# Kernel optimization log

Hardware: AMD Instinct MI355X
Metric: run time of the kernel (lower is better)

## Reference

```python
import jax, jax.numpy as jnp
import numpy as np

B, N_Z, NOISE_DIM, STATE_DIM, HIDDEN_DIM, CLASS_NUM = 2048, 8, 32, 1024, 1024, 1
EPI_HIDDEN = 512
PRIOR_H = 5
IN_FEATURES = NOISE_DIM + STATE_DIM + HIDDEN_DIM  # 2080
OUT_FEATURES = NOISE_DIM * CLASS_NUM  # 32
POSTERIOR_SCALE = 1.0
PRIOR_SCALE = 1.0


def _xavier(key, shape):
    fan_in, fan_out = shape[-2], shape[-1]
    std = np.sqrt(2.0 / (fan_in + fan_out)).astype(np.float32)
    return jax.random.normal(key, shape, dtype=jnp.float32) * std


def setup_inputs() -> dict:
    key = jax.random.key(0)
    ks = jax.random.split(key, 10)
    x = jax.random.normal(ks[0], (B, STATE_DIM), dtype=jnp.float32)
    feature = jax.random.normal(ks[1], (B, HIDDEN_DIM), dtype=jnp.float32)
    z = jax.random.normal(ks[2], (B, N_Z, NOISE_DIM), dtype=jnp.float32)
    # epinet: Linear(IN_FEATURES->EPI_HIDDEN), ReLU, Linear(EPI_HIDDEN->OUT_FEATURES)
    Wep1 = _xavier(ks[3], (IN_FEATURES, EPI_HIDDEN))
    bep1 = jnp.zeros((EPI_HIDDEN,), dtype=jnp.float32)
    Wep2 = _xavier(ks[4], (EPI_HIDDEN, OUT_FEATURES))
    bep2 = jnp.zeros((OUT_FEATURES,), dtype=jnp.float32)
    # priornet: ensemble of NOISE_DIM MLPs state_dim->5->5->class_num (frozen)
    Wp1 = _xavier(ks[5], (NOISE_DIM, STATE_DIM, PRIOR_H))
    bp1 = jnp.zeros((NOISE_DIM, PRIOR_H), dtype=jnp.float32)
    Wp2 = _xavier(ks[6], (NOISE_DIM, PRIOR_H, PRIOR_H))
    bp2 = jnp.zeros((NOISE_DIM, PRIOR_H), dtype=jnp.float32)
    Wp3 = _xavier(ks[7], (NOISE_DIM, PRIOR_H, CLASS_NUM))
    bp3 = jnp.zeros((NOISE_DIM, CLASS_NUM), dtype=jnp.float32)
    return {"x": x, "feature": feature, "z": z,
            "Wep1": Wep1, "bep1": bep1, "Wep2": Wep2, "bep2": bep2,
            "Wp1": Wp1, "bp1": bp1, "Wp2": Wp2, "bp2": bp2, "Wp3": Wp3, "bp3": bp3}


def reference(x, feature, z, Wep1, bep1, Wep2, bep2, Wp1, bp1, Wp2, bp2, Wp3, bp3):
    batch = x.shape[0]
    n = z.shape[1]
    # [B, state+hidden] -> broadcast over n z-samples, concat z -> [B, n, IN_FEATURES]
    xf = jnp.concatenate([x, feature], axis=-1)
    epinet_inp = jnp.concatenate(
        [jnp.broadcast_to(xf[:, None, :], (batch, n, xf.shape[-1])), z], axis=-1)
    # small epinet MLP
    h = jax.nn.relu(jnp.einsum('bnd,dh->bnh', epinet_inp, Wep1) + bep1)
    out = jnp.einsum('bnh,ho->bno', h, Wep2) + bep2  # [B, n, noise_dim*class_num]
    out = out.reshape(batch, n, NOISE_DIM, CLASS_NUM)
    out = jnp.einsum('bsna,bsn->bsa', out, z)  # [B, n, class_num]
    # ensemble prior: NOISE_DIM tiny MLPs, vectorized as batched GEMMs
    h1 = jax.nn.relu(jnp.einsum('bi,eih->beh', x, Wp1) + bp1)
    h2 = jax.nn.relu(jnp.einsum('beh,ehg->beg', h1, Wp2) + bp2)
    p = jnp.einsum('beg,egc->bec', h2, Wp3) + bp3  # [B, ensemble=noise_dim, class_num]
    prior_out = jnp.einsum('bzc,bnz->bnc', p, z)  # [B, n, class_num]
    return out * POSTERIOR_SCALE + prior_out * PRIOR_SCALE
```

## Files before the change

### kernel.cpp

```cpp
#include <hip/hip_runtime.h>
#include <hip/hip_bf16.h>


typedef __hip_bfloat16 bf16;
typedef __attribute__((ext_vector_type(8))) short short8;
typedef __attribute__((ext_vector_type(4))) float f32x4;

#define NCOMB 768
#define NSPLIT 8
#define A_BYTES   (2048u * 2048u * 2u)
#define WT_BYTES  (768u * 2048u * 2u)
#define WZT_BYTES (512u * 32u * 2u)
#define W2T_BYTES (32u * 512u * 2u)

__device__ __forceinline__ void gload_lds16(const bf16* g, bf16* l) {
    __builtin_amdgcn_global_load_lds(
        (const __attribute__((address_space(1))) void*)g,
        (__attribute__((address_space(3))) void*)l, 16, 0, 0);
}

__device__ __forceinline__ short f2bf_bits(float f) {
    bf16 h = __float2bfloat16(f);
    return *reinterpret_cast<short*>(&h);
}

__global__ __launch_bounds__(256) void prep(const float* __restrict__ x,
                                            const float* __restrict__ feat,
                                            const float* __restrict__ Wep1,
                                            const float* __restrict__ Wep2,
                                            const float* __restrict__ Wp1,
                                            bf16* __restrict__ A,
                                            bf16* __restrict__ WT,
                                            bf16* __restrict__ WzT,
                                            bf16* __restrict__ W2T) {
    const int t = threadIdx.x;
    const int blk = blockIdx.x;
    if (blk < 4096) {
        int idx = blk * 256 + t;
        int b = idx >> 9;
        int g = idx & 511;
        const float* src = (g < 256) ? (x + (size_t)b * 1024 + g * 4)
                                     : (feat + (size_t)b * 1024 + (g - 256) * 4);
        float4 v = *(const float4*)src;
        short4 p;
        p.x = f2bf_bits(v.x); p.y = f2bf_bits(v.y);
        p.z = f2bf_bits(v.z); p.w = f2bf_bits(v.w);
        *(short4*)(A + (size_t)b * 2048 + g * 4) = p;
    } else if (blk < 6400) {
        int wb = blk - 4096;
        if (wb < 256) {
            __shared__ short tile[64 * 66];
            int kt = wb >> 3, nt = wb & 7;
            int k0 = kt * 64, n0 = nt * 64;
            int r = t >> 4, cq = t & 15;
#pragma unroll
            for (int i = 0; i < 4; ++i) {
                int rr = r + i * 16;
                float4 v = *(const float4*)(Wep1 + (size_t)(k0 + rr) * 512 + n0 + cq * 4);
                tile[(cq * 4 + 0) * 66 + rr] = f2bf_bits(v.x);
                tile[(cq * 4 + 1) * 66 + rr] = f2bf_bits(v.y);
                tile[(cq * 4 + 2) * 66 + rr] = f2bf_bits(v.z);
                tile[(cq * 4 + 3) * 66 + rr] = f2bf_bits(v.w);
            }
            __syncthreads();
#pragma unroll
            for (int i = 0; i < 2; ++i) {
                int ch = i * 256 + t;
                int nr = ch >> 3, kc = ch & 7;
                short8 s = *(const short8*)(tile + nr * 66 + kc * 8);
                *(short8*)(WT + (size_t)(n0 + nr) * 2048 + k0 + kc * 8) = s;
            }
        } else {
            int local = (wb - 256) * 256 + t;
            int n = 512 + (local >> 11);
            int k = local & 2047;
            float v = 0.f;
            if (n < 672) {
                int q = n - 512;
                int e = q / 5, h = q - e * 5;
                if (k < 1024) v = Wp1[(size_t)e * 5120 + k * 5 + h];
            }
            WT[(size_t)n * 2048 + k] = __float2bfloat16(v);
        }
    } else if (blk < 6432) {
        int local = (blk - 6400) * 256 + t;
#pragma unroll
        for (int i = 0; i < 2; ++i) {
            int e = i * 8192 + local;
            int c = e >> 5, k = e & 31;
            WzT[e] = __float2bfloat16(Wep1[(size_t)(2048 + k) * 512 + c]);
        }
    } else {
        int local = (blk - 6432) * 256 + t;
#pragma unroll
        for (int i = 0; i < 2; ++i) {
            int e = i * 8192 + local;
            int j = e >> 9, c = e & 511;
            W2T[e] = __float2bfloat16(Wep2[(size_t)c * 32 + j]);
        }
    }
}

__global__ __launch_bounds__(256) void gemm_split(const bf16* __restrict__ A,
                                                  const bf16* __restrict__ WT,
                                                  float* __restrict__ Gp) {
    __shared__ bf16 As[128 * 64];
    __shared__ bf16 Bs[128 * 64];
    const int t    = threadIdx.x;
    const int lane = t & 63;
    const int wv   = t >> 6;
    const int m0 = blockIdx.x * 128;
    const int n0 = blockIdx.y * 128;
    const int kbase = blockIdx.z * 256;
    const int lm = lane & 15;
    const int lq = lane >> 4;
    const int wm = (wv & 1) * 64;
    const int wn = (wv >> 1) * 64;
    f32x4 acc[4][4] = {};

    for (int k0 = 0; k0 < 256; k0 += 64) {
        __syncthreads();
#pragma unroll
        for (int i = 0; i < 4; ++i) {
            int chunk = i * 256 + wv * 64 + lane;
            int row   = chunk >> 3;
            int gph   = chunk & 7;
            int gda   = gph ^ (row & 7);
            gload_lds16(A  + (size_t)(m0 + row) * 2048 + kbase + k0 + gda * 8,
                        As + (i * 256 + wv * 64) * 8);
            gload_lds16(WT + (size_t)(n0 + row) * 2048 + kbase + k0 + gda * 8,
                        Bs + (i * 256 + wv * 64) * 8);
        }
        __syncthreads();
#pragma unroll
        for (int kk = 0; kk < 64; kk += 32) {
            short8 af[4], bfr[4];
#pragma unroll
            for (int i2 = 0; i2 < 4; ++i2) {
                int ra = wm + i2 * 16 + lm;
                int ga = ((kk >> 3) + lq) ^ (ra & 7);
                af[i2] = *(const short8*)(As + ra * 64 + ga * 8);
                int rb = wn + i2 * 16 + lm;
                int gb = ((kk >> 3) + lq) ^ (rb & 7);
                bfr[i2] = *(const short8*)(Bs + rb * 64 + gb * 8);
            }
#pragma unroll
            for (int mi = 0; mi < 4; ++mi)
#pragma unroll
                for (int ni = 0; ni < 4; ++ni)
                    acc[mi][ni] = __builtin_amdgcn_mfma_f32_16x16x32_bf16(
                        af[mi], bfr[ni], acc[mi][ni], 0, 0, 0);
        }
    }
    const bool zhi = blockIdx.z >= 4;
    float* Gs = Gp + (size_t)blockIdx.z * 2048 * NCOMB;
#pragma unroll
    for (int mi = 0; mi < 4; ++mi)
#pragma unroll
        for (int ni = 0; ni < 4; ++ni) {
            int row = m0 + wm + mi * 16 + lq * 4;
            int col = n0 + wn + ni * 16 + lm;
            if (col < 672 && !(zhi && col >= 512)) {
#pragma unroll
                for (int r = 0; r < 4; ++r)
                    Gs[(size_t)(row + r) * NCOMB + col] = acc[mi][ni][r];
            }
        }
}

__global__ __launch_bounds__(256) void combine(const float* __restrict__ Gp,
                                               const float* __restrict__ z,
                                               const bf16* __restrict__ WzT,
                                               const bf16* __restrict__ W2T,
                                               const float* __restrict__ bep1,
                                               const float* __restrict__ bep2,
                                               const float* __restrict__ bp1,
                                               const float* __restrict__ Wp2,
                                               const float* __restrict__ bp2,
                                               const float* __restrict__ Wp3,
                                               const float* __restrict__ bp3,
                                               float* __restrict__ out) {
    __shared__ float zf[1024];
    __shared__ short zbf[1024];
    __shared__ float hxs[2048];
    __shared__ float h1s[640];
    __shared__ float h2s[640];
    __shared__ float ps[128];
    __shared__ short hB[32 * 512];
    __shared__ float o2s[1024];
    const int t = threadIdx.x, bg = blockIdx.x;
    const int lane = t & 63, wv = t >> 6;
    const int lm = lane & 15, lq = lane >> 4;
    const int mt = wv & 1;
    const int jt = wv >> 1;
    const size_t SSTR = (size_t)2048 * NCOMB;

    {
        float4 v = *(const float4*)(z + (size_t)bg * 1024 + t * 4);
        zf[t * 4 + 0] = v.x; zf[t * 4 + 1] = v.y; zf[t * 4 + 2] = v.z; zf[t * 4 + 3] = v.w;
        zbf[t * 4 + 0] = f2bf_bits(v.x); zbf[t * 4 + 1] = f2bf_bits(v.y);
        zbf[t * 4 + 2] = f2bf_bits(v.z); zbf[t * 4 + 3] = f2bf_bits(v.w);
    }
#pragma unroll
    for (int g = 0; g < 2; ++g) {
        int q = g * 256 + t;
        int bi = q >> 7, cq = q & 127;
        const float* gp = Gp + (size_t)(bg * 4 + bi) * NCOMB + cq * 4;
        float4 a4 = *(const float4*)(bep1 + cq * 4);
#pragma unroll
        for (int s = 0; s < 8; ++s) {
            float4 v = *(const float4*)(gp + (size_t)s * SSTR);
            a4.x += v.x; a4.y += v.y; a4.z += v.z; a4.w += v.w;
        }
        *(float4*)(hxs + bi * 512 + cq * 4) = a4;
    }
    if (t < 160) {
        float bv = bp1[t];
#pragma unroll
        for (int bi = 0; bi < 4; ++bi) {
            const float* gp = Gp + (size_t)(bg * 4 + bi) * NCOMB + 512 + t;
            float v = gp[0] + gp[SSTR] + gp[2 * SSTR] + gp[3 * SSTR] + bv;
            h1s[bi * 160 + t] = fmaxf(v, 0.f);
        }
    }
    __syncthreads();
    if (t < 160) {
        int e = t / 5, g5 = t - e * 5;
#pragma unroll
        for (int bi = 0; bi < 4; ++bi) {
            float a = bp2[t];
#pragma unroll
            for (int h = 0; h < 5; ++h)
                a += h1s[bi * 160 + e * 5 + h] * Wp2[e * 25 + h * 5 + g5];
            h2s[bi * 160 + t] = fmaxf(a, 0.f);
        }
    }
    __syncthreads();
    if (t < 128) {
        int bi = t >> 5, j = t & 31;
        float a = bp3[j];
#pragma unroll
        for (int g = 0; g < 5; ++g)
            a += h2s[bi * 160 + j * 5 + g] * Wp3[j * 5 + g];
        ps[bi * 32 + j] = a;
    }
    short8 afz = *(const short8*)(zbf + (mt * 16 + lm) * 32 + lq * 8);
#pragma unroll
    for (int u = 0; u < 16; ++u) {
        int crow = (jt * 16 + u) * 16 + lm;
        short8 bfz = *(const short8*)(WzT + crow * 32 + lq * 8);
        f32x4 az = {};
        az = __builtin_amdgcn_mfma_f32_16x16x32_bf16(afz, bfz, az, 0, 0, 0);
        int cg = crow >> 3, cl = crow & 7;
#pragma unroll
        for (int r = 0; r < 4; ++r) {
            int row = mt * 16 + lq * 4 + r;
            float hv = fmaxf(hxs[(row >> 3) * 512 + crow] + az[r], 0.f);
            hB[row * 512 + ((cg ^ row)) * 8 + cl] = f2bf_bits(hv);
        }
    }
    __syncthreads();
    f32x4 o2acc = {};
    {
        int arow = mt * 16 + lm;
        int jrow = jt * 16 + lm;
#pragma unroll
        for (int ks = 0; ks < 16; ++ks) {
            int dg = ks * 4 + lq;
            short8 a2 = *(const short8*)(hB + arow * 512 + (dg ^ arow) * 8);
            short8 b2 = *(const short8*)(W2T + jrow * 512 + dg * 8);
            o2acc = __builtin_amdgcn_mfma_f32_16x16x32_bf16(a2, b2, o2acc, 0, 0, 0);
        }
    }
#pragma unroll
    for (int r = 0; r < 4; ++r)
        o2s[(mt * 16 + lq * 4 + r) * 32 + jt * 16 + lm] = o2acc[r];
    __syncthreads();
    {
        int r = t >> 3, jg = t & 7;
        float val = 0.f;
#pragma unroll
        for (int u = 0; u < 4; ++u) {
            int j = jg * 4 + u;
            val += (o2s[r * 32 + j] + bep2[j] + ps[(r >> 3) * 32 + j]) * zf[r * 32 + j];
        }
        val += __shfl_xor(val, 1, 64);
        val += __shfl_xor(val, 2, 64);
        val += __shfl_xor(val, 4, 64);
        if ((t & 7) == 0) out[(size_t)bg * 32 + r] = val;
    }
}

extern "C" void kernel_launch(void* const* d_in, const int* in_sizes, int n_in,
                              void* d_out, int out_size, void* d_ws, size_t ws_size,
                              hipStream_t stream) {
    const float* x    = (const float*)d_in[0];
    const float* feat = (const float*)d_in[1];
    const float* z    = (const float*)d_in[2];
    const float* Wep1 = (const float*)d_in[3];
    const float* bep1 = (const float*)d_in[4];
    const float* Wep2 = (const float*)d_in[5];
    const float* bep2 = (const float*)d_in[6];
    const float* Wp1  = (const float*)d_in[7];
    const float* bp1  = (const float*)d_in[8];
    const float* Wp2  = (const float*)d_in[9];
    const float* bp2  = (const float*)d_in[10];
    const float* Wp3  = (const float*)d_in[11];
    const float* bp3  = (const float*)d_in[12];
    float* out = (float*)d_out;

    char* ws  = (char*)d_ws;
    bf16* A   = (bf16*)ws;
    bf16* WT  = (bf16*)(ws + A_BYTES);
    bf16* WzT = (bf16*)(ws + A_BYTES + WT_BYTES);
    bf16* W2T = (bf16*)(ws + A_BYTES + WT_BYTES + WZT_BYTES);
    float* Gp = (float*)(ws + A_BYTES + WT_BYTES + WZT_BYTES + W2T_BYTES);

    prep<<<6464, 256, 0, stream>>>(x, feat, Wep1, Wep2, Wp1, A, WT, WzT, W2T);
    gemm_split<<<dim3(16, 6, NSPLIT), 256, 0, stream>>>(A, WT, Gp);
    combine<<<512, 256, 0, stream>>>(Gp, z, WzT, W2T, bep1, bep2,
                                     bp1, Wp2, bp2, Wp3, bp3, out);
}
```

Measured before the change: 117.3 us.

## Skip zero-K prior tiles, store split-K partials as bf16, halve combine blocks

The split-K GEMM grid is flattened so the upper K splits launch only the four N-tiles that hold the epinet columns, and no blocks are spent on prior columns whose weights are zero over that K range. Prep no longer writes those zero halves of WT. Partial sums are stored in bf16 instead of fp32, which halves the write and read traffic between GEMM and combine. Combine now handles two batch rows per 128-thread block. Rounding partial sums to bf16 before the split-K reduction adds accumulation error.

```diff
diff --git a/kernel.cpp b/kernel.cpp
--- a/kernel.cpp
+++ b/kernel.cpp
@@ -7,11 +7,11 @@
 typedef __attribute__((ext_vector_type(4))) float f32x4;
 
 #define NCOMB 768
-#define NSPLIT 8
 #define A_BYTES   (2048u * 2048u * 2u)
 #define WT_BYTES  (768u * 2048u * 2u)
 #define WZT_BYTES (512u * 32u * 2u)
 #define W2T_BYTES (32u * 512u * 2u)
+#define GP_SSTR ((size_t)2048 * NCOMB)
 
 __device__ __forceinline__ void gload_lds16(const bf16* g, bf16* l) {
     __builtin_amdgcn_global_load_lds(
@@ -22,6 +22,9 @@
 __device__ __forceinline__ short f2bf_bits(float f) {
     bf16 h = __float2bfloat16(f);
     return *reinterpret_cast<short*>(&h);
+}
+__device__ __forceinline__ float bfu2f(unsigned short u) {
+    return __uint_as_float(((unsigned int)u) << 16);
 }
 
 __global__ __launch_bounds__(256) void prep(const float* __restrict__ x,
@@ -46,44 +49,42 @@
         p.x = f2bf_bits(v.x); p.y = f2bf_bits(v.y);
         p.z = f2bf_bits(v.z); p.w = f2bf_bits(v.w);
         *(short4*)(A + (size_t)b * 2048 + g * 4) = p;
-    } else if (blk < 6400) {
+    } else if (blk < 4352) {
+        __shared__ short tile[64 * 66];
         int wb = blk - 4096;
-        if (wb < 256) {
-            __shared__ short tile[64 * 66];
-            int kt = wb >> 3, nt = wb & 7;
-            int k0 = kt * 64, n0 = nt * 64;
-            int r = t >> 4, cq = t & 15;
-#pragma unroll
-            for (int i = 0; i < 4; ++i) {
-                int rr = r + i * 16;
-                float4 v = *(const float4*)(Wep1 + (size_t)(k0 + rr) * 512 + n0 + cq * 4);
-                tile[(cq * 4 + 0) * 66 + rr] = f2bf_bits(v.x);
-                tile[(cq * 4 + 1) * 66 + rr] = f2bf_bits(v.y);
-                tile[(cq * 4 + 2) * 66 + rr] = f2bf_bits(v.z);
-                tile[(cq * 4 + 3) * 66 + rr] = f2bf_bits(v.w);
-            }
-            __syncthreads();
-#pragma unroll
-            for (int i = 0; i < 2; ++i) {
-                int ch = i * 256 + t;
-                int nr = ch >> 3, kc = ch & 7;
-                short8 s = *(const short8*)(tile + nr * 66 + kc * 8);
-                *(short8*)(WT + (size_t)(n0 + nr) * 2048 + k0 + kc * 8) = s;
-            }
-        } else {
-            int local = (wb - 256) * 256 + t;
-            int n = 512 + (local >> 11);
-            int k = local & 2047;
-            float v = 0.f;
-            if (n < 672) {
-                int q = n - 512;
-                int e = q / 5, h = q - e * 5;
-                if (k < 1024) v = Wp1[(size_t)e * 5120 + k * 5 + h];
-            }
-            WT[(size_t)n * 2048 + k] = __float2bfloat16(v);
-        }
-    } else if (blk < 6432) {
-        int local = (blk - 6400) * 256 + t;
+        int kt = wb >> 3, nt = wb & 7;
+        int k0 = kt * 64, n0 = nt * 64;
+        int r = t >> 4, cq = t & 15;
+#pragma unroll
+        for (int i = 0; i < 4; ++i) {
+            int rr = r + i * 16;
+            float4 v = *(const float4*)(Wep1 + (size_t)(k0 + rr) * 512 + n0 + cq * 4);
+            tile[(cq * 4 + 0) * 66 + rr] = f2bf_bits(v.x);
+            tile[(cq * 4 + 1) * 66 + rr] = f2bf_bits(v.y);
+            tile[(cq * 4 + 2) * 66 + rr] = f2bf_bits(v.z);
+            tile[(cq * 4 + 3) * 66 + rr] = f2bf_bits(v.w);
+        }
+        __syncthreads();
+#pragma unroll
+        for (int i = 0; i < 2; ++i) {
+            int ch = i * 256 + t;
+            int nr = ch >> 3, kc = ch & 7;
+            short8 s = *(const short8*)(tile + nr * 66 + kc * 8);
+            *(short8*)(WT + (size_t)(n0 + nr) * 2048 + k0 + kc * 8) = s;
+        }
+    } else if (blk < 5376) {
+        int local = (blk - 4352) * 256 + t;
+        int n = 512 + (local >> 10);
+        int k = local & 1023;
+        float v = 0.f;
+        if (n < 672) {
+            int q = n - 512;
+            int e = q / 5, h = q - e * 5;
+            v = Wp1[(size_t)e * 5120 + k * 5 + h];
+        }
+        WT[(size_t)n * 2048 + k] = __float2bfloat16(v);
+    } else if (blk < 5408) {
+        int local = (blk - 5376) * 256 + t;
 #pragma unroll
         for (int i = 0; i < 2; ++i) {
             int e = i * 8192 + local;
@@ -91,7 +92,7 @@
             WzT[e] = __float2bfloat16(Wep1[(size_t)(2048 + k) * 512 + c]);
         }
     } else {
-        int local = (blk - 6432) * 256 + t;
+        int local = (blk - 5408) * 256 + t;
 #pragma unroll
         for (int i = 0; i < 2; ++i) {
             int e = i * 8192 + local;
@@ -103,15 +104,19 @@
 
 __global__ __launch_bounds__(256) void gemm_split(const bf16* __restrict__ A,
                                                   const bf16* __restrict__ WT,
-                                                  float* __restrict__ Gp) {
+                                                  bf16* __restrict__ Gp) {
     __shared__ bf16 As[128 * 64];
     __shared__ bf16 Bs[128 * 64];
     const int t    = threadIdx.x;
     const int lane = t & 63;
     const int wv   = t >> 6;
+    const int y = blockIdx.y;
+    int s, ny;
+    if (y < 24) { s = y / 6; ny = y - s * 6; }
+    else        { int q = y - 24; s = 4 + (q >> 2); ny = q & 3; }
     const int m0 = blockIdx.x * 128;
-    const int n0 = blockIdx.y * 128;
-    const int kbase = blockIdx.z * 256;
+    const int n0 = ny * 128;
+    const int kbase = s * 256;
     const int lm = lane & 15;
     const int lq = lane >> 4;
     const int wm = (wv & 1) * 64;
@@ -152,23 +157,23 @@
                         af[mi], bfr[ni], acc[mi][ni], 0, 0, 0);
         }
     }
-    const bool zhi = blockIdx.z >= 4;
-    float* Gs = Gp + (size_t)blockIdx.z * 2048 * NCOMB;
+    bf16* Gs = Gp + (size_t)s * GP_SSTR;
+    const bool full = (s >= 4);
 #pragma unroll
     for (int mi = 0; mi < 4; ++mi)
 #pragma unroll
         for (int ni = 0; ni < 4; ++ni) {
             int row = m0 + wm + mi * 16 + lq * 4;
             int col = n0 + wn + ni * 16 + lm;
-            if (col < 672 && !(zhi && col >= 512)) {
+            if (full || col < 672) {
 #pragma unroll
                 for (int r = 0; r < 4; ++r)
-                    Gs[(size_t)(row + r) * NCOMB + col] = acc[mi][ni][r];
+                    Gs[(size_t)(row + r) * NCOMB + col] = __float2bfloat16(acc[mi][ni][r]);
             }
         }
 }
 
-__global__ __launch_bounds__(256) void combine(const float* __restrict__ Gp,
+__global__ __launch_bounds__(128) void combine(const bf16* __restrict__ Gp,
                                                const float* __restrict__ z,
                                                const bf16* __restrict__ WzT,
                                                const bf16* __restrict__ W2T,
@@ -180,63 +185,61 @@
                                                const float* __restrict__ Wp3,
                                                const float* __restrict__ bp3,
                                                float* __restrict__ out) {
-    __shared__ float zf[1024];
-    __shared__ short zbf[1024];
-    __shared__ float hxs[2048];
-    __shared__ float h1s[640];
-    __shared__ float h2s[640];
-    __shared__ float ps[128];
-    __shared__ short hB[32 * 512];
-    __shared__ float o2s[1024];
+    __shared__ float zf[512];
+    __shared__ short zbf[512];
+    __shared__ float hxs[1024];
+    __shared__ float h1s[320];
+    __shared__ float h2s[320];
+    __shared__ float ps[64];
+    __shared__ short hB[16 * 512];
+    __shared__ float o2s[512];
     const int t = threadIdx.x, bg = blockIdx.x;
-    const int lane = t & 63, wv = t >> 6;
+    const int b0 = bg * 2;
+    const int lane = t & 63;
+    const int jt = t >> 6;
     const int lm = lane & 15, lq = lane >> 4;
-    const int mt = wv & 1;
-    const int jt = wv >> 1;
-    const size_t SSTR = (size_t)2048 * NCOMB;
 
     {
-        float4 v = *(const float4*)(z + (size_t)bg * 1024 + t * 4);
+        float4 v = *(const float4*)(z + (size_t)b0 * 256 + t * 4);
         zf[t * 4 + 0] = v.x; zf[t * 4 + 1] = v.y; zf[t * 4 + 2] = v.z; zf[t * 4 + 3] = v.w;
         zbf[t * 4 + 0] = f2bf_bits(v.x); zbf[t * 4 + 1] = f2bf_bits(v.y);
         zbf[t * 4 + 2] = f2bf_bits(v.z); zbf[t * 4 + 3] = f2bf_bits(v.w);
     }
 #pragma unroll
     for (int g = 0; g < 2; ++g) {
-        int q = g * 256 + t;
+        int q = g * 128 + t;
         int bi = q >> 7, cq = q & 127;
-        const float* gp = Gp + (size_t)(bg * 4 + bi) * NCOMB + cq * 4;
+        const unsigned short* gp =
+            (const unsigned short*)(Gp + (size_t)(b0 + bi) * NCOMB + cq * 4);
         float4 a4 = *(const float4*)(bep1 + cq * 4);
 #pragma unroll
         for (int s = 0; s < 8; ++s) {
-            float4 v = *(const float4*)(gp + (size_t)s * SSTR);
-            a4.x += v.x; a4.y += v.y; a4.z += v.z; a4.w += v.w;
+            ushort4 v = *(const ushort4*)(gp + (size_t)s * GP_SSTR);
+            a4.x += bfu2f(v.x); a4.y += bfu2f(v.y);
+            a4.z += bfu2f(v.z); a4.w += bfu2f(v.w);
         }
         *(float4*)(hxs + bi * 512 + cq * 4) = a4;
     }
-    if (t < 160) {
-        float bv = bp1[t];
-#pragma unroll
-        for (int bi = 0; bi < 4; ++bi) {
-            const float* gp = Gp + (size_t)(bg * 4 + bi) * NCOMB + 512 + t;
-            float v = gp[0] + gp[SSTR] + gp[2 * SSTR] + gp[3 * SSTR] + bv;
-            h1s[bi * 160 + t] = fmaxf(v, 0.f);
-        }
+    for (int e = t; e < 320; e += 128) {
+        int bi = (e >= 160), c = e - bi * 160;
+        const unsigned short* gp =
+            (const unsigned short*)(Gp + (size_t)(b0 + bi) * NCOMB + 512 + c);
+        float v = bp1[c] + bfu2f(gp[0]) + bfu2f(gp[GP_SSTR])
+                + bfu2f(gp[2 * GP_SSTR]) + bfu2f(gp[3 * GP_SSTR]);
+        h1s[e] = fmaxf(v, 0.f);
     }
     __syncthreads();
-    if (t < 160) {
-        int e = t / 5, g5 = t - e * 5;
-#pragma unroll
-        for (int bi = 0; bi < 4; ++bi) {
-            float a = bp2[t];
-#pragma unroll
-            for (int h = 0; h < 5; ++h)
-                a += h1s[bi * 160 + e * 5 + h] * Wp2[e * 25 + h * 5 + g5];
-            h2s[bi * 160 + t] = fmaxf(a, 0.f);
-        }
+    for (int e = t; e < 320; e += 128) {
+        int bi = (e >= 160), c = e - bi * 160;
+        int en = c / 5, g5 = c - en * 5;
+        float a = bp2[c];
+#pragma unroll
+        for (int h = 0; h < 5; ++h)
+            a += h1s[bi * 160 + en * 5 + h] * Wp2[en * 25 + h * 5 + g5];
+        h2s[e] = fmaxf(a, 0.f);
     }
     __syncthreads();
-    if (t < 128) {
+    if (t < 64) {
         int bi = t >> 5, j = t & 31;
         float a = bp3[j];
 #pragma unroll
@@ -244,37 +247,36 @@
             a += h2s[bi * 160 + j * 5 + g] * Wp3[j * 5 + g];
         ps[bi * 32 + j] = a;
     }
-    short8 afz = *(const short8*)(zbf + (mt * 16 + lm) * 32 + lq * 8);
+    short8 afz = *(const short8*)(zbf + lm * 32 + lq * 8);
 #pragma unroll
     for (int u = 0; u < 16; ++u) {
-        int crow = (jt * 16 + u) * 16 + lm;
+        int crow = jt * 256 + u * 16 + lm;
         short8 bfz = *(const short8*)(WzT + crow * 32 + lq * 8);
         f32x4 az = {};
         az = __builtin_amdgcn_mfma_f32_16x16x32_bf16(afz, bfz, az, 0, 0, 0);
         int cg = crow >> 3, cl = crow & 7;
 #pragma unroll
         for (int r = 0; r < 4; ++r) {
-            int row = mt * 16 + lq * 4 + r;
+            int row = lq * 4 + r;
             float hv = fmaxf(hxs[(row >> 3) * 512 + crow] + az[r], 0.f);
-            hB[row * 512 + ((cg ^ row)) * 8 + cl] = f2bf_bits(hv);
+            hB[row * 512 + (cg ^ row) * 8 + cl] = f2bf_bits(hv);
         }
     }
     __syncthreads();
     f32x4 o2acc = {};
     {
-        int arow = mt * 16 + lm;
         int jrow = jt * 16 + lm;
 #pragma unroll
         for (int ks = 0; ks < 16; ++ks) {
             int dg = ks * 4 + lq;
-            short8 a2 = *(const short8*)(hB + arow * 512 + (dg ^ arow) * 8);
+            short8 a2 = *(const short8*)(hB + lm * 512 + (dg ^ lm) * 8);
             short8 b2 = *(const short8*)(W2T + jrow * 512 + dg * 8);
             o2acc = __builtin_amdgcn_mfma_f32_16x16x32_bf16(a2, b2, o2acc, 0, 0, 0);
         }
     }
 #pragma unroll
     for (int r = 0; r < 4; ++r)
-        o2s[(mt * 16 + lq * 4 + r) * 32 + jt * 16 + lm] = o2acc[r];
+        o2s[(lq * 4 + r) * 32 + jt * 16 + lm] = o2acc[r];
     __syncthreads();
     {
         int r = t >> 3, jg = t & 7;
@@ -287,7 +289,7 @@
         val += __shfl_xor(val, 1, 64);
         val += __shfl_xor(val, 2, 64);
         val += __shfl_xor(val, 4, 64);
-        if ((t & 7) == 0) out[(size_t)bg * 32 + r] = val;
+        if ((t & 7) == 0) out[(size_t)bg * 16 + r] = val;
     }
 }
 
@@ -314,10 +316,10 @@
     bf16* WT  = (bf16*)(ws + A_BYTES);
     bf16* WzT = (bf16*)(ws + A_BYTES + WT_BYTES);
     bf16* W2T = (bf16*)(ws + A_BYTES + WT_BYTES + WZT_BYTES);
-    float* Gp = (float*)(ws + A_BYTES + WT_BYTES + WZT_BYTES + W2T_BYTES);
-
-    prep<<<6464, 256, 0, stream>>>(x, feat, Wep1, Wep2, Wp1, A, WT, WzT, W2T);
-    gemm_split<<<dim3(16, 6, NSPLIT), 256, 0, stream>>>(A, WT, Gp);
-    combine<<<512, 256, 0, stream>>>(Gp, z, WzT, W2T, bep1, bep2,
-                                     bp1, Wp2, bp2, Wp3, bp3, out);
-}
+    bf16* Gp  = (bf16*)(ws + A_BYTES + WT_BYTES + WZT_BYTES + W2T_BYTES);
+
+    prep<<<5440, 256, 0, stream>>>(x, feat, Wep1, Wep2, Wp1, A, WT, WzT, W2T);
+    gemm_split<<<dim3(16, 40), 256, 0, stream>>>(A, WT, Gp);
+    combine<<<1024, 128, 0, stream>>>(Gp, z, WzT, W2T, bep1, bep2,
+                                      bp1, Wp2, bp2, Wp3, bp3, out);
+}
```

After: 117.4 us. Within noise of the previous version (+0.1%).
